# Performance work log

Measured on AMD Instinct MI355X. Metric: run time of the kernel, lower is better.

## Reference

```python
import jax, jax.numpy as jnp
import numpy as np

EMBED_DIM = 1024
EXPAND_RATIO = 128  # head_dim; n_heads = EMBED_DIM // EXPAND_RATIO = 8
B, N = 4, 2048


def setup_inputs() -> dict:
    key = jax.random.key(0)
    ks = jax.random.split(key, 6)
    std = 0.02
    d = EMBED_DIM
    return {
        "x": jax.random.normal(ks[0], (B, N, d), dtype=jnp.float32),
        "Wq": jax.random.normal(ks[1], (d, d), dtype=jnp.float32) * std,
        "Wk": jax.random.normal(ks[2], (d, d), dtype=jnp.float32) * std,
        "Wv": jax.random.normal(ks[3], (d, d), dtype=jnp.float32) * std,
        "Wo": jax.random.normal(ks[4], (d, d), dtype=jnp.float32) * std,
        "norm_w": jnp.ones((d,), dtype=jnp.float32),
    }


def _rmsnorm(x, w, eps=1e-6):
    return x * jax.lax.rsqrt(jnp.mean(x * x, axis=-1, keepdims=True) + eps) * w


def _gla_scan(q, k, v, g):
    # q,k,v,g: [b, n, h, d]; state S: [b, h, d_k, d_v]
    b, n, h, d = q.shape
    qs, ks_, vs, gs = (jnp.moveaxis(t, 1, 0) for t in (q, k, v, g))  # [n,b,h,d]
    S0 = jnp.zeros((b, h, d, d), dtype=q.dtype)

    def step(S, inp):
        q_t, k_t, v_t, g_t = inp
        # S_t = diag(exp(g_t)) S_{t-1} + k_t^T v_t (gate on key dim)
        S = jnp.exp(g_t)[..., :, None] * S + k_t[..., :, None] * v_t[..., None, :]
        o_t = jnp.einsum('bhk,bhkv->bhv', q_t, S)
        return S, o_t

    _, outs = jax.lax.scan(step, S0, (qs, ks_, vs, gs))
    return jnp.moveaxis(outs, 0, 1)  # [b, n, h, d]


def reference(x, Wq, Wk, Wv, Wo, norm_w):
    b, n, D = x.shape
    hd = EXPAND_RATIO
    h = D // hd

    q = jax.nn.silu(x @ Wq.T)          # q_activation = silu
    f = jax.nn.sigmoid(x @ Wk.T)       # f = sigmoid(k_proj(x))
    log_f = jax.nn.log_sigmoid(f)      # faithful: logsigmoid applied to f (lower_bound=None path)
    k = 1.0 - f
    v = x @ Wv.T

    def split_heads(t):
        return t.reshape(b, n, h, hd)

    out = _gla_scan(split_heads(q), split_heads(k), split_heads(v), split_heads(log_f))
    out = out.reshape(b, n, D)
    out = _rmsnorm(out, norm_w)        # norm_pos='ogate', no output gate
    return out @ Wo.T
```

## Files before the change

kernel.cpp:

```cpp
#include <hip/hip_runtime.h>
#include <cstdint>
#include <cstddef>


typedef unsigned short u16;
using f32x4  = __attribute__((ext_vector_type(4))) float;
using bf16x8 = __attribute__((ext_vector_type(8))) short;

__device__ __forceinline__ float bf2f(u16 u) {
  union { unsigned int i; float f; } v; v.i = ((unsigned int)u) << 16; return v.f;
}
__device__ __forceinline__ u16 f2bf(float f) {
  union { float f; unsigned int i; } v; v.f = f;
  unsigned int r = v.i + 0x7fffu + ((v.i >> 16) & 1u);
  return (u16)(r >> 16);
}
__device__ __forceinline__ void async_load16(const void* g, void* l) {
  __builtin_amdgcn_global_load_lds(
      (const __attribute__((address_space(1))) unsigned int*)(uintptr_t)g,
      (__attribute__((address_space(3))) unsigned int*)(uintptr_t)l, 16, 0, 0);
}

__device__ __forceinline__ void gemm128_core(const u16* __restrict__ Ag, const u16* __restrict__ Bg,
                                             u16* smem, f32x4 (&acc)[4][4]) {
  const int tid = threadIdx.x;
  const int lane = tid & 63, wave = tid >> 6;
  const int wm = (wave & 1) * 64, wn = (wave >> 1) * 64;
  const int r = lane & 15, quad = lane >> 4;
  const int xk = r & 3;
  const u16* baseA = smem + (wm + r) * 32 + ((quad ^ xk) & 3) * 8;
  const u16* baseB = smem + 4096 + (wn + r) * 32 + ((quad ^ xk) & 3) * 8;
  const int soff = (tid >> 2) * 1024 + (((tid & 3) ^ ((tid >> 2) & 3)) * 8);
  u16* dA = smem + wave * 512;
  u16* dB = smem + 4096 + wave * 512;
#pragma unroll
  for (int it = 0; it < 2; ++it) {
    async_load16(Ag + it * 65536 + soff, dA + it * 2048);
    async_load16(Bg + it * 65536 + soff, dB + it * 2048);
  }
#pragma unroll 2
  for (int kt = 0; kt < 32; ++kt) {
    const int cb = (kt & 1) * 8192;
    __syncthreads();
    if (kt < 31) {
      const int nb = ((kt + 1) & 1) * 8192;
      const u16* As = Ag + (kt + 1) * 32 + soff;
      const u16* Bs = Bg + (kt + 1) * 32 + soff;
#pragma unroll
      for (int it = 0; it < 2; ++it) {
        async_load16(As + it * 65536, dA + nb + it * 2048);
        async_load16(Bs + it * 65536, dB + nb + it * 2048);
      }
    }
    bf16x8 af[4], bv[4];
#pragma unroll
    for (int i = 0; i < 4; ++i) af[i] = *(const bf16x8*)(baseA + cb + i * 512);
#pragma unroll
    for (int j = 0; j < 4; ++j) bv[j] = *(const bf16x8*)(baseB + cb + j * 512);
#pragma unroll
    for (int i = 0; i < 4; ++i)
#pragma unroll
      for (int j = 0; j < 4; ++j)
        acc[i][j] = __builtin_amdgcn_mfma_f32_16x16x32_bf16(af[i], bv[j], acc[i][j], 0, 0, 0);
  }
}

__global__ __launch_bounds__(256) void cast_f32_bf16(const float* __restrict__ src,
                                                     u16* __restrict__ dst, int n4) {
  int i = blockIdx.x * 256 + threadIdx.x;
  if (i >= n4) return;
  float4 v = ((const float4*)src)[i];
  unsigned int lo = (unsigned)f2bf(v.x) | ((unsigned)f2bf(v.y) << 16);
  unsigned int hi = (unsigned)f2bf(v.z) | ((unsigned)f2bf(v.w) << 16);
  ((uint2*)dst)[i] = make_uint2(lo, hi);
}

__global__ __launch_bounds__(256) void cast_w4(const float* __restrict__ w0, const float* __restrict__ w1,
                                               const float* __restrict__ w2, const float* __restrict__ w3,
                                               const float* __restrict__ nw,
                                               u16* __restrict__ d0, u16* __restrict__ d1,
                                               u16* __restrict__ d2, u16* __restrict__ d3) {
  const float* src = blockIdx.y == 0 ? w0 : (blockIdx.y == 1 ? w1 : (blockIdx.y == 2 ? w2 : w3));
  u16* dst = blockIdx.y == 0 ? d0 : (blockIdx.y == 1 ? d1 : (blockIdx.y == 2 ? d2 : d3));
  int i = blockIdx.x * 256 + threadIdx.x;
  float4 v = ((const float4*)src)[i];
  if (blockIdx.y == 3) {
    float4 wv = ((const float4*)nw)[i & 255];
    v.x *= wv.x; v.y *= wv.y; v.z *= wv.z; v.w *= wv.w;
  }
  unsigned int lo = (unsigned)f2bf(v.x) | ((unsigned)f2bf(v.y) << 16);
  unsigned int hi = (unsigned)f2bf(v.z) | ((unsigned)f2bf(v.w) << 16);
  ((uint2*)dst)[i] = make_uint2(lo, hi);
}

__global__ __launch_bounds__(256) void hgru_gemm_qkv(
    const u16* __restrict__ Xb, const u16* __restrict__ Wqb, const u16* __restrict__ Wkb,
    const u16* __restrict__ Wvb, u16* __restrict__ Qb, u16* __restrict__ Kb,
    u16* __restrict__ Vb) {
  __shared__ alignas(16) u16 smem[16384];
  const int which = blockIdx.y >> 3, bn = blockIdx.y & 7;
  const u16* W = which == 0 ? Wqb : (which == 1 ? Wkb : Wvb);
  const u16* Ag = Xb + (size_t)blockIdx.x * 128 * 1024;
  const u16* Bg = W + (size_t)bn * 128 * 1024;
  f32x4 acc[4][4] = {};
  gemm128_core(Ag, Bg, smem, acc);
  const int tid = threadIdx.x, lane = tid & 63, wave = tid >> 6;
  const int wm = (wave & 1) * 64, wn = (wave >> 1) * 64;
  const int r = lane & 15, quad = lane >> 4;
#pragma unroll
  for (int i = 0; i < 4; ++i)
#pragma unroll
    for (int j = 0; j < 4; ++j)
#pragma unroll
      for (int reg = 0; reg < 4; ++reg) {
        int m = blockIdx.x * 128 + wm + i * 16 + quad * 4 + reg;
        int n = bn * 128 + wn + j * 16 + r;
        size_t off = (size_t)m * 1024 + n;
        float z = acc[i][j][reg];
        if (which == 0) {
          Qb[off] = f2bf(z / (1.f + __expf(-z)));
        } else if (which == 1) {
          float ek = __expf(-z);
          Kb[off] = f2bf(ek / (1.f + ek));
        } else {
          Vb[off] = f2bf(z);
        }
      }
}

__global__ __launch_bounds__(256) void hgru_scan(
    const u16* __restrict__ Qg, const u16* __restrict__ Kg, const u16* __restrict__ Vg,
    u16* __restrict__ O) {
  __shared__ alignas(16) char smem[42496];
  float* sb  = (float*)(smem);
  u16* sU    = (u16*)(smem);
  u16* sKt   = (u16*)(smem + 17408);
  u16* sVt1  = (u16*)(smem + 27648);
  u16* sQ    = (u16*)(smem + 17408);
  u16* sK    = (u16*)(smem + 26112);
  u16* sVt2  = (u16*)(smem + 34816);
  u16* sAm   = (u16*)(smem + 39936);

  const int tid = threadIdx.x, blk = blockIdx.x;
  const int vh = blk & 1, c = (blk >> 1) & 63, bh = blk >> 7, h = bh & 7, bb_ = bh >> 3;
  const size_t rb = (size_t)(bb_ * 2048 + c * 32) * 1024 + h * 128;
  const bool haveP = (c > 0);
  const size_t rb1 = haveP ? rb - 32 * 1024 : rb;

  const int lane = tid & 63, wave = tid >> 6;
  const int r = lane & 15, quad = lane >> 4;
  const int ts = tid & 31;
  const int g8 = tid >> 5;

  uint4 Q2[2], K2[2], K1[2], V2, V1;
#pragma unroll
  for (int it = 0; it < 2; ++it) {
    Q2[it] = *(const uint4*)(Qg + rb  + (size_t)ts * 1024 + (it * 8 + g8) * 8);
    K2[it] = *(const uint4*)(Kg + rb  + (size_t)ts * 1024 + (it * 8 + g8) * 8);
    K1[it] = *(const uint4*)(Kg + rb1 + (size_t)ts * 1024 + (it * 8 + g8) * 8);
  }
  V2 = *(const uint4*)(Vg + rb  + (size_t)ts * 1024 + vh * 64 + g8 * 8);
  V1 = *(const uint4*)(Vg + rb1 + (size_t)ts * 1024 + vh * 64 + g8 * 8);

  f32x4 accU[2][4] = {};
  const int vm = (wave & 1) * 32, in = (wave >> 1) * 64;

  if (haveP) {
    { const int col = tid & 127, half = tid >> 7;
      float run = 0.f;
      const size_t gb = rb1 + (size_t)(half * 16) * 1024 + col;
#pragma unroll
      for (int t = 0; t < 16; ++t) {
        float kv = bf2f(Kg[gb + (size_t)t * 1024]);
        run -= __logf(1.f + __expf(-(1.f - kv)));
        sb[(half * 16 + t) * 129 + col] = run;
      } }
    __syncthreads();
    { if (tid >> 7) { const int col = tid & 127; float fix = sb[15 * 129 + col];
#pragma unroll
        for (int t = 16; t < 32; ++t) sb[t * 129 + col] += fix; } }
    __syncthreads();
#pragma unroll
    for (int it = 0; it < 2; ++it) {
      const int i8 = it * 8 + g8;
      const u16* kp = (const u16*)&K1[it];
#pragma unroll
      for (int e = 0; e < 8; ++e) {
        int i = i8 * 8 + e;
        float bs = sb[ts * 129 + i];
        float bC = sb[31 * 129 + i];
        sKt[i * 40 + ts] = f2bf(bf2f(kp[e]) * __expf(bC - bs));
      }
    }
    { const u16* vp = (const u16*)&V1;
#pragma unroll
      for (int e = 0; e < 8; ++e) sVt1[(g8 * 8 + e) * 40 + ts] = vp[e]; }
    __syncthreads();
#pragma unroll
    for (int mi = 0; mi < 2; ++mi) {
      bf16x8 af = *(const bf16x8*)(sVt1 + (vm + mi * 16 + r) * 40 + quad * 8);
#pragma unroll
      for (int nj = 0; nj < 4; ++nj) {
        bf16x8 bv = *(const bf16x8*)(sKt + (in + nj * 16 + r) * 40 + quad * 8);
        accU[mi][nj] = __builtin_amdgcn_mfma_f32_16x16x32_bf16(af, bv, accU[mi][nj], 0, 0, 0);
      }
    }
  }
  { const int col = tid & 127, half = tid >> 7;
    float run = 0.f;
    const size_t gb = rb + (size_t)(half * 16) * 1024 + col;
#pragma unroll
    for (int t = 0; t < 16; ++t) {
      float kv = bf2f(Kg[gb + (size_t)t * 1024]);
      run -= __logf(1.f + __expf(-(1.f - kv)));
      sb[(half * 16 + t) * 129 + col] = run;
    } }
  __syncthreads();
  { if (tid >> 7) { const int col = tid & 127; float fix = sb[15 * 129 + col];
#pragma unroll
      for (int t = 16; t < 32; ++t) sb[t * 129 + col] += fix; } }
  __syncthreads();
#pragma unroll
  for (int it = 0; it < 2; ++it) {
    const int i8 = it * 8 + g8;
    const u16* qp = (const u16*)&Q2[it];
    const u16* kp = (const u16*)&K2[it];
    u16 qo[8], ko[8];
#pragma unroll
    for (int e = 0; e < 8; ++e) {
      int i = i8 * 8 + e;
      float bt = sb[ts * 129 + i];
      qo[e] = f2bf(bf2f(qp[e]) * __expf(bt));
      ko[e] = f2bf(bf2f(kp[e]) * __expf(-bt));
    }
    *(uint4*)(sQ + ts * 136 + i8 * 8) = *(const uint4*)qo;
    *(uint4*)(sK + ts * 136 + i8 * 8) = *(const uint4*)ko;
  }
  { const u16* vp = (const u16*)&V2;
#pragma unroll
    for (int e = 0; e < 8; ++e) sVt2[(g8 * 8 + e) * 40 + ts] = vp[e]; }
  __syncthreads();
  { const int mi = wave & 1, nj = wave >> 1;
    f32x4 a1 = {0.f, 0.f, 0.f, 0.f};
#pragma unroll
    for (int ks = 0; ks < 4; ++ks) {
      bf16x8 af = *(const bf16x8*)(sQ + (mi * 16 + r) * 136 + ks * 32 + quad * 8);
      bf16x8 bk = *(const bf16x8*)(sK + (nj * 16 + r) * 136 + ks * 32 + quad * 8);
      a1 = __builtin_amdgcn_mfma_f32_16x16x32_bf16(af, bk, a1, 0, 0, 0);
    }
#pragma unroll
    for (int reg = 0; reg < 4; ++reg) {
      int t = mi * 16 + quad * 4 + reg, s = nj * 16 + r;
      sAm[t * 40 + s] = (s <= t) ? f2bf(a1[reg]) : (u16)0;
    } }
  if (haveP) {
#pragma unroll
    for (int mi = 0; mi < 2; ++mi)
#pragma unroll
      for (int nj = 0; nj < 4; ++nj)
#pragma unroll
        for (int reg = 0; reg < 4; ++reg) {
          int vl = vm + mi * 16 + quad * 4 + reg;
          int i  = in + nj * 16 + r;
          sU[vl * 136 + i] = f2bf(accU[mi][nj][reg]);
        }
  }
  __syncthreads();
  { const int mi = wave & 1, no = (wave >> 1) * 32;
    bf16x8 af0 = *(const bf16x8*)(sAm + (mi * 16 + r) * 40 + quad * 8);
    bf16x8 afq[4];
    if (haveP) {
#pragma unroll
      for (int ks = 0; ks < 4; ++ks)
        afq[ks] = *(const bf16x8*)(sQ + (mi * 16 + r) * 136 + ks * 32 + quad * 8);
    }
#pragma unroll
    for (int j = 0; j < 2; ++j) {
      f32x4 acc2 = {0.f, 0.f, 0.f, 0.f};
      bf16x8 bv0 = *(const bf16x8*)(sVt2 + (no + j * 16 + r) * 40 + quad * 8);
      acc2 = __builtin_amdgcn_mfma_f32_16x16x32_bf16(af0, bv0, acc2, 0, 0, 0);
      if (haveP) {
#pragma unroll
        for (int ks = 0; ks < 4; ++ks) {
          bf16x8 bs = *(const bf16x8*)(sU + (no + j * 16 + r) * 136 + ks * 32 + quad * 8);
          acc2 = __builtin_amdgcn_mfma_f32_16x16x32_bf16(afq[ks], bs, acc2, 0, 0, 0);
        }
      }
#pragma unroll
      for (int reg = 0; reg < 4; ++reg) {
        int t = mi * 16 + quad * 4 + reg;
        int vg = vh * 64 + no + j * 16 + r;
        O[rb + (size_t)t * 1024 + vg] = f2bf(acc2[reg]);
      }
    } }
}

__global__ __launch_bounds__(256) void hgru_sumsq(const u16* __restrict__ O,
                                                  float* __restrict__ s) {
  const int row = blockIdx.x * 4 + (threadIdx.x >> 6);
  const int lane = threadIdx.x & 63;
  const u16* p = O + (size_t)row * 1024 + lane * 16;
  uint4 a = *(const uint4*)p;
  uint4 b = *(const uint4*)(p + 8);
  float ss = 0.f;
  const unsigned int* w = (const unsigned int*)&a;
#pragma unroll
  for (int e = 0; e < 4; ++e) {
    float lo = bf2f((u16)(w[e] & 0xffff)), hi = bf2f((u16)(w[e] >> 16));
    ss += lo * lo + hi * hi;
  }
  const unsigned int* w2 = (const unsigned int*)&b;
#pragma unroll
  for (int e = 0; e < 4; ++e) {
    float lo = bf2f((u16)(w2[e] & 0xffff)), hi = bf2f((u16)(w2[e] >> 16));
    ss += lo * lo + hi * hi;
  }
#pragma unroll
  for (int m = 32; m >= 1; m >>= 1) ss += __shfl_xor(ss, m);
  if (lane == 0) s[row] = rsqrtf(ss * (1.f / 1024.f) + 1e-6f);
}

__global__ __launch_bounds__(256) void hgru_gemm_out(const u16* __restrict__ Ab,
                                                     const u16* __restrict__ Wob,
                                                     const float* __restrict__ s,
                                                     float* __restrict__ out) {
  __shared__ alignas(16) u16 smem[16384];
  const u16* Ag = Ab + (size_t)blockIdx.x * 128 * 1024;
  const u16* Bg = Wob + (size_t)blockIdx.y * 128 * 1024;
  f32x4 acc[4][4] = {};
  gemm128_core(Ag, Bg, smem, acc);
  const int tid = threadIdx.x, lane = tid & 63, wave = tid >> 6;
  const int wm = (wave & 1) * 64, wn = (wave >> 1) * 64;
  const int r = lane & 15, quad = lane >> 4;
#pragma unroll
  for (int i = 0; i < 4; ++i)
#pragma unroll
    for (int reg = 0; reg < 4; ++reg) {
      int m = blockIdx.x * 128 + wm + i * 16 + quad * 4 + reg;
      float sm = s[m];
#pragma unroll
      for (int j = 0; j < 4; ++j) {
        int n = blockIdx.y * 128 + wn + j * 16 + r;
        out[(size_t)m * 1024 + n] = acc[i][j][reg] * sm;
      }
    }
}

extern "C" void kernel_launch(void* const* d_in, const int* in_sizes, int n_in,
                              void* d_out, int out_size, void* d_ws, size_t ws_size,
                              hipStream_t stream) {
  const float* x  = (const float*)d_in[0];
  const float* Wq = (const float*)d_in[1];
  const float* Wk = (const float*)d_in[2];
  const float* Wv = (const float*)d_in[3];
  const float* Wo = (const float*)d_in[4];
  const float* nw = (const float*)d_in[5];
  float* out = (float*)d_out;
  char* ws = (char*)d_ws;

  u16* Xb   = (u16*)(ws + 0);
  u16* Wqb  = (u16*)(ws + 16777216);
  u16* Wkb  = (u16*)(ws + 18874368);
  u16* Wvb  = (u16*)(ws + 20971520);
  u16* Wob  = (u16*)(ws + 23068672);
  u16* Qb   = (u16*)(ws + 25165824);
  u16* Kb   = (u16*)(ws + 41943040);
  u16* Vb   = (u16*)(ws + 58720256);
  u16* Obf  = (u16*)(ws + 75497472);
  float* Sv = (float*)(ws + 92274688);

  cast_f32_bf16<<<8192, 256, 0, stream>>>(x, Xb, 2097152);
  dim3 gw(1024, 4);
  cast_w4<<<gw, 256, 0, stream>>>(Wq, Wk, Wv, Wo, nw, Wqb, Wkb, Wvb, Wob);

  dim3 gq(64, 24);
  hgru_gemm_qkv<<<gq, 256, 0, stream>>>(Xb, Wqb, Wkb, Wvb, Qb, Kb, Vb);
  hgru_scan<<<4096, 256, 0, stream>>>(Qb, Kb, Vb, Obf);
  hgru_sumsq<<<2048, 256, 0, stream>>>(Obf, Sv);
  dim3 go(64, 8);
  hgru_gemm_out<<<go, 256, 0, stream>>>(Obf, Wob, Sv, out);
}
```

Baseline: 239.5 us.

## Fuse casts, fold RMS sum-of-squares into scan, narrow output GEMM tiles

Merges the x and weight cast kernels into one launch. The separate sum-of-squares kernel is removed: the scan kernel now accumulates per-row squared outputs with shuffle reductions and atomics into a buffer that is zeroed by a memset. The output GEMM computes rsqrt from those sums and switches to 128x64 tiles, giving 1024 blocks for better CU occupancy. The trade-offs are float atomic contention, sums taken from fp32 values rather than the rounded bf16 values, and less data reuse per output tile.

```diff
diff --git a/kernel.cpp b/kernel.cpp
--- a/kernel.cpp
+++ b/kernel.cpp
@@ -65,26 +65,67 @@
   }
 }
 
-__global__ __launch_bounds__(256) void cast_f32_bf16(const float* __restrict__ src,
-                                                     u16* __restrict__ dst, int n4) {
-  int i = blockIdx.x * 256 + threadIdx.x;
-  if (i >= n4) return;
+__device__ __forceinline__ void gemm64_core(const u16* __restrict__ Ag, const u16* __restrict__ Bg,
+                                            u16* smem, f32x4 (&acc)[4][2]) {
+  const int tid = threadIdx.x;
+  const int lane = tid & 63, wave = tid >> 6;
+  const int wm = (wave & 1) * 64, wn = (wave >> 1) * 32;
+  const int r = lane & 15, quad = lane >> 4;
+  const int xk = r & 3;
+  const u16* baseA = smem + (wm + r) * 32 + ((quad ^ xk) & 3) * 8;
+  const u16* baseB = smem + 4096 + (wn + r) * 32 + ((quad ^ xk) & 3) * 8;
+  const int soff = (tid >> 2) * 1024 + (((tid & 3) ^ ((tid >> 2) & 3)) * 8);
+  u16* dA = smem + wave * 512;
+  u16* dB = smem + 4096 + wave * 512;
+#pragma unroll
+  for (int it = 0; it < 2; ++it) async_load16(Ag + it * 65536 + soff, dA + it * 2048);
+  async_load16(Bg + soff, dB);
+#pragma unroll 2
+  for (int kt = 0; kt < 32; ++kt) {
+    const int cb = (kt & 1) * 6144;
+    __syncthreads();
+    if (kt < 31) {
+      const int nb = ((kt + 1) & 1) * 6144;
+      const u16* As = Ag + (kt + 1) * 32 + soff;
+      const u16* Bs = Bg + (kt + 1) * 32 + soff;
+#pragma unroll
+      for (int it = 0; it < 2; ++it) async_load16(As + it * 65536, dA + nb + it * 2048);
+      async_load16(Bs, dB + nb);
+    }
+    bf16x8 af[4], bv[2];
+#pragma unroll
+    for (int i = 0; i < 4; ++i) af[i] = *(const bf16x8*)(baseA + cb + i * 512);
+#pragma unroll
+    for (int j = 0; j < 2; ++j) bv[j] = *(const bf16x8*)(baseB + cb + j * 512);
+#pragma unroll
+    for (int i = 0; i < 4; ++i)
+#pragma unroll
+      for (int j = 0; j < 2; ++j)
+        acc[i][j] = __builtin_amdgcn_mfma_f32_16x16x32_bf16(af[i], bv[j], acc[i][j], 0, 0, 0);
+  }
+}
+
+__global__ __launch_bounds__(256) void cast_all(
+    const float* __restrict__ x, const float* __restrict__ w0, const float* __restrict__ w1,
+    const float* __restrict__ w2, const float* __restrict__ w3, const float* __restrict__ nw,
+    u16* __restrict__ xd, u16* __restrict__ d0, u16* __restrict__ d1,
+    u16* __restrict__ d2, u16* __restrict__ d3) {
+  const int blk = blockIdx.x;
+  const float* src;
+  u16* dst;
+  int i;
+  bool fold = false;
+  if (blk < 8192) {
+    src = x; dst = xd; i = blk * 256 + threadIdx.x;
+  } else {
+    int wb = blk - 8192, which = wb >> 10;
+    i = (wb & 1023) * 256 + threadIdx.x;
+    src = which == 0 ? w0 : (which == 1 ? w1 : (which == 2 ? w2 : w3));
+    dst = which == 0 ? d0 : (which == 1 ? d1 : (which == 2 ? d2 : d3));
+    fold = (which == 3);
+  }
   float4 v = ((const float4*)src)[i];
-  unsigned int lo = (unsigned)f2bf(v.x) | ((unsigned)f2bf(v.y) << 16);
-  unsigned int hi = (unsigned)f2bf(v.z) | ((unsigned)f2bf(v.w) << 16);
-  ((uint2*)dst)[i] = make_uint2(lo, hi);
-}
-
-__global__ __launch_bounds__(256) void cast_w4(const float* __restrict__ w0, const float* __restrict__ w1,
-                                               const float* __restrict__ w2, const float* __restrict__ w3,
-                                               const float* __restrict__ nw,
-                                               u16* __restrict__ d0, u16* __restrict__ d1,
-                                               u16* __restrict__ d2, u16* __restrict__ d3) {
-  const float* src = blockIdx.y == 0 ? w0 : (blockIdx.y == 1 ? w1 : (blockIdx.y == 2 ? w2 : w3));
-  u16* dst = blockIdx.y == 0 ? d0 : (blockIdx.y == 1 ? d1 : (blockIdx.y == 2 ? d2 : d3));
-  int i = blockIdx.x * 256 + threadIdx.x;
-  float4 v = ((const float4*)src)[i];
-  if (blockIdx.y == 3) {
+  if (fold) {
     float4 wv = ((const float4*)nw)[i & 255];
     v.x *= wv.x; v.y *= wv.y; v.z *= wv.z; v.w *= wv.w;
   }
@@ -130,7 +171,7 @@
 
 __global__ __launch_bounds__(256) void hgru_scan(
     const u16* __restrict__ Qg, const u16* __restrict__ Kg, const u16* __restrict__ Vg,
-    u16* __restrict__ O) {
+    u16* __restrict__ O, float* __restrict__ Ssum) {
   __shared__ alignas(16) char smem[42496];
   float* sb  = (float*)(smem);
   u16* sU    = (u16*)(smem);
@@ -274,6 +315,7 @@
       for (int ks = 0; ks < 4; ++ks)
         afq[ks] = *(const bf16x8*)(sQ + (mi * 16 + r) * 136 + ks * 32 + quad * 8);
     }
+    f32x4 ssq = {0.f, 0.f, 0.f, 0.f};
 #pragma unroll
     for (int j = 0; j < 2; ++j) {
       f32x4 acc2 = {0.f, 0.f, 0.f, 0.f};
@@ -286,61 +328,45 @@
           acc2 = __builtin_amdgcn_mfma_f32_16x16x32_bf16(afq[ks], bs, acc2, 0, 0, 0);
         }
       }
+      ssq += acc2 * acc2;
 #pragma unroll
       for (int reg = 0; reg < 4; ++reg) {
         int t = mi * 16 + quad * 4 + reg;
         int vg = vh * 64 + no + j * 16 + r;
         O[rb + (size_t)t * 1024 + vg] = f2bf(acc2[reg]);
       }
+    }
+    const int rowg = bb_ * 2048 + c * 32 + mi * 16 + quad * 4;
+#pragma unroll
+    for (int reg = 0; reg < 4; ++reg) {
+      float v = ssq[reg];
+      v += __shfl_xor(v, 1); v += __shfl_xor(v, 2);
+      v += __shfl_xor(v, 4); v += __shfl_xor(v, 8);
+      if (r == 0) atomicAdd(&Ssum[rowg + reg], v);
     } }
-}
-
-__global__ __launch_bounds__(256) void hgru_sumsq(const u16* __restrict__ O,
-                                                  float* __restrict__ s) {
-  const int row = blockIdx.x * 4 + (threadIdx.x >> 6);
-  const int lane = threadIdx.x & 63;
-  const u16* p = O + (size_t)row * 1024 + lane * 16;
-  uint4 a = *(const uint4*)p;
-  uint4 b = *(const uint4*)(p + 8);
-  float ss = 0.f;
-  const unsigned int* w = (const unsigned int*)&a;
-#pragma unroll
-  for (int e = 0; e < 4; ++e) {
-    float lo = bf2f((u16)(w[e] & 0xffff)), hi = bf2f((u16)(w[e] >> 16));
-    ss += lo * lo + hi * hi;
-  }
-  const unsigned int* w2 = (const unsigned int*)&b;
-#pragma unroll
-  for (int e = 0; e < 4; ++e) {
-    float lo = bf2f((u16)(w2[e] & 0xffff)), hi = bf2f((u16)(w2[e] >> 16));
-    ss += lo * lo + hi * hi;
-  }
-#pragma unroll
-  for (int m = 32; m >= 1; m >>= 1) ss += __shfl_xor(ss, m);
-  if (lane == 0) s[row] = rsqrtf(ss * (1.f / 1024.f) + 1e-6f);
 }
 
 __global__ __launch_bounds__(256) void hgru_gemm_out(const u16* __restrict__ Ab,
                                                      const u16* __restrict__ Wob,
-                                                     const float* __restrict__ s,
+                                                     const float* __restrict__ Ssum,
                                                      float* __restrict__ out) {
-  __shared__ alignas(16) u16 smem[16384];
+  __shared__ alignas(16) u16 smem[12288];
   const u16* Ag = Ab + (size_t)blockIdx.x * 128 * 1024;
-  const u16* Bg = Wob + (size_t)blockIdx.y * 128 * 1024;
-  f32x4 acc[4][4] = {};
-  gemm128_core(Ag, Bg, smem, acc);
+  const u16* Bg = Wob + (size_t)blockIdx.y * 64 * 1024;
+  f32x4 acc[4][2] = {};
+  gemm64_core(Ag, Bg, smem, acc);
   const int tid = threadIdx.x, lane = tid & 63, wave = tid >> 6;
-  const int wm = (wave & 1) * 64, wn = (wave >> 1) * 64;
+  const int wm = (wave & 1) * 64, wn = (wave >> 1) * 32;
   const int r = lane & 15, quad = lane >> 4;
 #pragma unroll
   for (int i = 0; i < 4; ++i)
 #pragma unroll
     for (int reg = 0; reg < 4; ++reg) {
       int m = blockIdx.x * 128 + wm + i * 16 + quad * 4 + reg;
-      float sm = s[m];
-#pragma unroll
-      for (int j = 0; j < 4; ++j) {
-        int n = blockIdx.y * 128 + wn + j * 16 + r;
+      float sm = rsqrtf(Ssum[m] * (1.f / 1024.f) + 1e-6f);
+#pragma unroll
+      for (int j = 0; j < 2; ++j) {
+        int n = blockIdx.y * 64 + wn + j * 16 + r;
         out[(size_t)m * 1024 + n] = acc[i][j][reg] * sm;
       }
     }
@@ -369,14 +395,12 @@
   u16* Obf  = (u16*)(ws + 75497472);
   float* Sv = (float*)(ws + 92274688);
 
-  cast_f32_bf16<<<8192, 256, 0, stream>>>(x, Xb, 2097152);
-  dim3 gw(1024, 4);
-  cast_w4<<<gw, 256, 0, stream>>>(Wq, Wk, Wv, Wo, nw, Wqb, Wkb, Wvb, Wob);
+  cast_all<<<12288, 256, 0, stream>>>(x, Wq, Wk, Wv, Wo, nw, Xb, Wqb, Wkb, Wvb, Wob);
+  hipMemsetAsync(Sv, 0, 8192 * sizeof(float), stream);
 
   dim3 gq(64, 24);
   hgru_gemm_qkv<<<gq, 256, 0, stream>>>(Xb, Wqb, Wkb, Wvb, Qb, Kb, Vb);
-  hgru_scan<<<4096, 256, 0, stream>>>(Qb, Kb, Vb, Obf);
-  hgru_sumsq<<<2048, 256, 0, stream>>>(Obf, Sv);
-  dim3 go(64, 8);
+  hgru_scan<<<4096, 256, 0, stream>>>(Qb, Kb, Vb, Obf, Sv);
+  dim3 go(64, 16);
   hgru_gemm_out<<<go, 256, 0, stream>>>(Obf, Wob, Sv, out);
 }
```

Result: slower. 245.8 us (+2.6%).
